# Kernel optimization log

Measured on AMD Instinct MI355X. Metric: run time of the kernel, lower is better.

Reference implementation:

```python
import jax, jax.numpy as jnp
import numpy as np

B, T, D, H, L = 4, 2048, 256, 4, 2
HD = D // H
VOCAB, MAX_BITS, MLP_H = 32, 64, 64


def setup_inputs() -> dict:
    key = jax.random.key(0)
    ks = jax.random.split(key, 20)
    s = 0.02
    n = lambda k, shp: (jax.random.normal(k, shp, jnp.float32) * s)
    inp = {
        'tokens': jax.random.randint(ks[0], (B, T), 0, VOCAB),
        'embed': n(ks[1], (VOCAB, D)),
        'ln1_w': jnp.ones((L, D)), 'ln1_b': jnp.zeros((L, D)),
        'qkv_w': n(ks[2], (L, D, 3 * D)), 'qkv_b': jnp.zeros((L, 3 * D)),
        'proj_w': n(ks[3], (L, D, D)), 'proj_b': jnp.zeros((L, D)),
        'ln2_w': jnp.ones((L, D)), 'ln2_b': jnp.zeros((L, D)),
        'ffn1_w': n(ks[4], (L, D, 4 * D)), 'ffn1_b': jnp.zeros((L, 4 * D)),
        'ffn2_w': n(ks[5], (L, 4 * D, D)), 'ffn2_b': jnp.zeros((L, D)),
        'lnf_w': jnp.ones((D,)), 'lnf_b': jnp.zeros((D,)),
        'out_queries': n(ks[6], (MAX_BITS * 2, D)),
        'outp_w': n(ks[7], (D, 1)), 'outp_b': jnp.zeros((1,)),
        'mlp_w1': n(ks[8], (3, MLP_H)), 'mlp_b1': jnp.zeros((MLP_H,)),
        'mlp_w2': n(ks[9], (MLP_H, MLP_H)), 'mlp_b2': jnp.zeros((MLP_H,)),
        'mlp_w3': n(ks[10], (MLP_H, 2)), 'mlp_b3': jnp.zeros((2,)),
    }
    return inp


def _layernorm(x, w, b, eps=1e-5):
    mu = jnp.mean(x, axis=-1, keepdims=True)
    var = jnp.mean(jnp.square(x - mu), axis=-1, keepdims=True)
    return (x - mu) * jax.lax.rsqrt(var + eps) * w + b


def _rope_tables(t_len, hd):
    inv_freq = 1.0 / (10000.0 ** (jnp.arange(0, hd, 2, dtype=jnp.float32) / hd))
    freqs = jnp.outer(jnp.arange(t_len, dtype=jnp.float32), inv_freq)  # [T, hd/2]
    emb = jnp.concatenate([freqs, freqs], axis=-1)                     # [T, hd]
    return jnp.cos(emb)[None, :, None, :], jnp.sin(emb)[None, :, None, :]


def _rotate_half(x):
    x1, x2 = x[..., : x.shape[-1] // 2], x[..., x.shape[-1] // 2:]
    return jnp.concatenate([-x2, x1], axis=-1)


def _attention(x, qkv_w, qkv_b, proj_w, proj_b):
    b, t, c = x.shape
    qkv = (x @ qkv_w + qkv_b).reshape(b, t, 3, H, HD)
    q, k, v = qkv[:, :, 0], qkv[:, :, 1], qkv[:, :, 2]  # [B,T,H,HD]
    cos, sin = _rope_tables(t, HD)
    q = q * cos + _rotate_half(q) * sin
    k = k * cos + _rotate_half(k) * sin
    scores = jnp.einsum('bthd,bshd->bhts', q, k) / jnp.sqrt(jnp.float32(HD))
    causal = jnp.tril(jnp.ones((t, t), dtype=bool))
    scores = jnp.where(causal, scores, -jnp.inf)
    attn = jax.nn.softmax(scores, axis=-1)
    out = jnp.einsum('bhts,bshd->bthd', attn, v).reshape(b, t, c)
    return out @ proj_w + proj_b


def reference(tokens, embed, ln1_w, ln1_b, qkv_w, qkv_b, proj_w, proj_b,
              ln2_w, ln2_b, ffn1_w, ffn1_b, ffn2_w, ffn2_b, lnf_w, lnf_b,
              out_queries, outp_w, outp_b,
              mlp_w1, mlp_b1, mlp_w2, mlp_b2, mlp_w3, mlp_b3):
    x = embed[tokens]  # [B,T,D]
    for l in range(L):
        x = x + _attention(_layernorm(x, ln1_w[l], ln1_b[l]),
                           qkv_w[l], qkv_b[l], proj_w[l], proj_b[l])
        h = _layernorm(x, ln2_w[l], ln2_b[l])
        h = jax.nn.gelu(h @ ffn1_w[l] + ffn1_b[l], approximate=False)
        x = x + (h @ ffn2_w[l] + ffn2_b[l])
    x = _layernorm(x, lnf_w, lnf_b)
    # query cross-attention for bit-pair selection
    q_scores = jnp.einsum('qd,btd->bqt', out_queries, x) / jnp.sqrt(jnp.float32(D))
    q_attn = jax.nn.softmax(q_scores, axis=-1)           # [B, 2*MAX_BITS, T]
    selected = jnp.einsum('bqt,btd->bqd', q_attn, x)
    bits = jax.nn.sigmoid((selected @ outp_w + outp_b)[..., 0])
    pairs = bits.reshape(-1, MAX_BITS, 2)                # [B, MAX_BITS, 2]

    # sequential full-adder over bits
    def step(carry, ab):  # carry [B], ab [B,2]
        z = jnp.concatenate([ab, carry[:, None]], axis=-1)  # [B,3]
        h = jax.nn.relu(z @ mlp_w1 + mlp_b1)
        h = jax.nn.relu(h @ mlp_w2 + mlp_b2)
        o = jax.nn.sigmoid(h @ mlp_w3 + mlp_b3)
        return o[:, 1], o[:, 0]

    carry0 = jnp.zeros((pairs.shape[0],), jnp.float32)
    carry, sum_bits = jax.lax.scan(step, carry0, jnp.swapaxes(pairs, 0, 1))
    sum_all = jnp.concatenate([sum_bits.T, carry[:, None]], axis=1)  # [B, MAX_BITS+1]
    return sum_all, pairs, q_attn
```

## Files before the change

kernel.cpp:

```cpp
#include <hip/hip_runtime.h>
#include <hip/hip_bf16.h>

#define BB 4
#define TT 2048
#define DD 256
#define HH 4
#define HDD 64
#define NROW 8192
#define NQ 128

typedef __hip_bfloat16 bf16;
typedef __attribute__((ext_vector_type(8))) short bf8v;
typedef __attribute__((ext_vector_type(4))) short bf4v;
typedef __attribute__((ext_vector_type(4))) float f4v;
typedef __attribute__((ext_vector_type(2))) unsigned int u2v;

__device__ __forceinline__ bf16 f2b(float v){ return __float2bfloat16(v); }
__device__ __forceinline__ short f2bs(float v){
    bf16 h = __float2bfloat16(v);
    return *reinterpret_cast<short*>(&h);
}
__device__ __forceinline__ float bs2f(short s){
    bf16 h = *reinterpret_cast<bf16*>(&s);
    return __bfloat162float(h);
}
__device__ __forceinline__ float rl(float v, int l){
    return __uint_as_float(__builtin_amdgcn_readlane(__float_as_uint(v), l));
}

#define DPP_ROR_ADD(v, ctrl) \
    ((v) + __int_as_float(__builtin_amdgcn_update_dpp(0, __float_as_int(v), (ctrl), 0xF, 0xF, false)))
#define DPP_ROR_MAX(v, ctrl) \
    fmaxf((v), __int_as_float(__builtin_amdgcn_update_dpp(0, __float_as_int(v), (ctrl), 0xF, 0xF, false)))

__device__ __forceinline__ void plswap16(float v, float& a, float& b){
#if __has_builtin(__builtin_amdgcn_permlane16_swap)
    u2v r = __builtin_amdgcn_permlane16_swap(__float_as_uint(v), __float_as_uint(v), false, false);
    a = __uint_as_float(r.x); b = __uint_as_float(r.y);
#else
    a = v; b = v;
    asm volatile("" : "+v"(b));
    asm("v_permlane16_swap_b32 %0, %1" : "+v"(a), "+v"(b));
#endif
}
__device__ __forceinline__ void plswap32(float v, float& a, float& b){
#if __has_builtin(__builtin_amdgcn_permlane32_swap)
    u2v r = __builtin_amdgcn_permlane32_swap(__float_as_uint(v), __float_as_uint(v), false, false);
    a = __uint_as_float(r.x); b = __uint_as_float(r.y);
#else
    a = v; b = v;
    asm volatile("" : "+v"(b));
    asm("v_permlane32_swap_b32 %0, %1" : "+v"(a), "+v"(b));
#endif
}
__device__ __forceinline__ float swap16_add(float v){ float a,b; plswap16(v,a,b); return a + b; }
__device__ __forceinline__ float swap32_add(float v){ float a,b; plswap32(v,a,b); return a + b; }
__device__ __forceinline__ float swap16_max(float v){ float a,b; plswap16(v,a,b); return fmaxf(a,b); }
__device__ __forceinline__ float swap32_max(float v){ float a,b; plswap32(v,a,b); return fmaxf(a,b); }
__device__ __forceinline__ float wsum(float v){
    v = DPP_ROR_ADD(v, 0x121); v = DPP_ROR_ADD(v, 0x122);
    v = DPP_ROR_ADD(v, 0x124); v = DPP_ROR_ADD(v, 0x128);
    v = swap16_add(v); v = swap32_add(v);
    return v;
}
__device__ __forceinline__ float wmax(float v){
    v = DPP_ROR_MAX(v, 0x121); v = DPP_ROR_MAX(v, 0x122);
    v = DPP_ROR_MAX(v, 0x124); v = DPP_ROR_MAX(v, 0x128);
    v = swap16_max(v); v = swap32_max(v);
    return v;
}

#define MFMA32(A,B,C) __builtin_amdgcn_mfma_f32_16x16x32_bf16((A),(B),(C),0,0,0)
#if __has_builtin(__builtin_amdgcn_mfma_f32_16x16x16bf16_1k)
#define MFMA16(A,B,C) __builtin_amdgcn_mfma_f32_16x16x16bf16_1k((A),(B),(C),0,0,0)
#else
__device__ __forceinline__ f4v mfma16_asm(bf4v a, bf4v b, f4v c){
    f4v d;
    asm("v_mfma_f32_16x16x16_bf16 %0, %1, %2, %3" : "=v"(d) : "v"(a), "v"(b), "v"(c));
    return d;
}
#define MFMA16(A,B,C) mfma16_asm((A),(B),(C))
#endif

__global__ __launch_bounds__(256) void k_embln(const int* __restrict__ tok,
                                               const float* __restrict__ emb,
                                               const float* __restrict__ w,
                                               const float* __restrict__ b,
                                               float* __restrict__ x,
                                               bf16* __restrict__ Y){
    int row = blockIdx.x*4 + (threadIdx.x >> 6);
    int lane = threadIdx.x & 63;
    f4v v = *(const f4v*)(emb + (long)tok[row]*DD + lane*4);
    *(f4v*)(x + (long)row*DD + lane*4) = v;
    float s  = (v[0]+v[1]) + (v[2]+v[3]);
    float s2 = (v[0]*v[0]+v[1]*v[1]) + (v[2]*v[2]+v[3]*v[3]);
    s = wsum(s); s2 = wsum(s2);
    float mu  = s * (1.0f/DD);
    float var = s2 * (1.0f/DD) - mu*mu;
    float rs  = rsqrtf(var + 1e-5f);
    f4v wv4 = *(const f4v*)(w + lane*4);
    f4v bv4 = *(const f4v*)(b + lane*4);
    bf4v o;
    #pragma unroll
    for (int i=0;i<4;i++) o[i] = f2bs((v[i]-mu)*rs*wv4[i] + bv4[i]);
    *(bf4v*)(Y + (long)row*DD + lane*4) = o;
}

__global__ __launch_bounds__(256) void k_misc(const float* __restrict__ oq, bf16* __restrict__ oqb,
                                              float* __restrict__ cosT, float* __restrict__ sinT,
                                              const float* __restrict__ w2, float* __restrict__ w2t){
    int gid = blockIdx.x*256 + threadIdx.x;
    {
        int t = gid >> 5, dd = gid & 31;
        float invf = powf(10000.0f, -(float)(2*dd)/64.0f);
        float ang = (float)t * invf;
        float sn, cs;
        sincosf(ang, &sn, &cs);
        cosT[gid] = cs; sinT[gid] = sn;
    }
    if (gid < NQ*DD) oqb[gid] = f2b(oq[gid]);
    if (gid < 4096){ int j = gid >> 6, k = gid & 63; w2t[gid] = w2[k*64 + j]; }
}

__global__ __launch_bounds__(256) void k_wtall(const float* __restrict__ qkvw,
                                               const float* __restrict__ projw,
                                               const float* __restrict__ f1w,
                                               const float* __restrict__ f2w,
                                               bf16* __restrict__ wt){
    __shared__ float t[32][33];
    int z = blockIdx.z;
    int l = z >> 2, type = z & 3;
    long L = (long)l*786432;
    int K, M; const float* src; long doff;
    if (type == 0){ K=256;  M=768;  src = qkvw + (long)l*256*768;  doff = L; }
    else if (type == 1){ K=256;  M=256;  src = projw + (long)l*256*256; doff = L + 196608; }
    else if (type == 2){ K=256;  M=1024; src = f1w  + (long)l*256*1024; doff = L + 262144; }
    else               { K=1024; M=256;  src = f2w  + (long)l*1024*256; doff = L + 524288; }
    int m0 = blockIdx.x*32, k0 = blockIdx.y*32;
    if (m0 >= M || k0 >= K) return;
    bf16* dst = wt + doff;
    int tx = threadIdx.x, ty = threadIdx.y;
    #pragma unroll
    for (int i=0;i<4;i++)
        t[ty+i*8][tx] = src[(long)(k0+ty+i*8)*M + m0 + tx];
    __syncthreads();
    #pragma unroll
    for (int i=0;i<4;i++)
        dst[(long)(m0+ty+i*8)*K + k0 + tx] = f2b(t[tx][ty+i*8]);
}

__global__ __launch_bounds__(256) void k_lnb(const float* __restrict__ X,
                                             const float* __restrict__ w,
                                             const float* __restrict__ b,
                                             bf16* __restrict__ Y){
    int row = blockIdx.x*4 + (threadIdx.x >> 6);
    int lane = threadIdx.x & 63;
    f4v v = *(const f4v*)(X + (long)row*DD + lane*4);
    float s  = (v[0]+v[1]) + (v[2]+v[3]);
    float s2 = (v[0]*v[0]+v[1]*v[1]) + (v[2]*v[2]+v[3]*v[3]);
    s = wsum(s); s2 = wsum(s2);
    float mu  = s * (1.0f/DD);
    float var = s2 * (1.0f/DD) - mu*mu;
    float rs  = rsqrtf(var + 1e-5f);
    f4v wv4 = *(const f4v*)(w + lane*4);
    f4v bv4 = *(const f4v*)(b + lane*4);
    bf4v o;
    #pragma unroll
    for (int i=0;i<4;i++) o[i] = f2bs((v[i]-mu)*rs*wv4[i] + bv4[i]);
    *(bf4v*)(Y + (long)row*DD + lane*4) = o;
}

__global__ __launch_bounds__(256) void k_lnf(const float* __restrict__ X,
                                             const float* __restrict__ w,
                                             const float* __restrict__ b,
                                             const float* __restrict__ ow,
                                             bf16* __restrict__ Yb,
                                             float* __restrict__ g){
    int row = blockIdx.x*4 + (threadIdx.x >> 6);
    int lane = threadIdx.x & 63;
    f4v v = *(const f4v*)(X + (long)row*DD + lane*4);
    float s  = (v[0]+v[1]) + (v[2]+v[3]);
    float s2 = (v[0]*v[0]+v[1]*v[1]) + (v[2]*v[2]+v[3]*v[3]);
    s = wsum(s); s2 = wsum(s2);
    float mu  = s * (1.0f/DD);
    float var = s2 * (1.0f/DD) - mu*mu;
    float rs  = rsqrtf(var + 1e-5f);
    f4v wv4 = *(const f4v*)(w + lane*4);
    f4v bv4 = *(const f4v*)(b + lane*4);
    f4v ov4 = *(const f4v*)(ow + lane*4);
    bf4v o;
    float gp = 0.f;
    #pragma unroll
    for (int i=0;i<4;i++){
        float y = (v[i]-mu)*rs*wv4[i] + bv4[i];
        o[i] = f2bs(y);
        gp += y * ov4[i];
    }
    *(bf4v*)(Yb + (long)row*DD + lane*4) = o;
    gp = wsum(gp);
    if (lane == 0) g[row] = gp;
}

__global__ __launch_bounds__(256) void k_mgemm(const bf16* __restrict__ A,
                                               const bf16* __restrict__ Wt,
                                               const float* __restrict__ bias,
                                               float* __restrict__ Cf,
                                               bf16* __restrict__ Cb,
                                               int K, int M, int mode){
    __shared__ short As[128*64];
    __shared__ short Ws[64*64];
    int tid = threadIdx.x;
    int lane = tid & 63, wv = tid >> 6;
    int n0 = blockIdx.y * 128, m0 = blockIdx.x * 64;
    int rbase = (wv >> 1) * 64, cbase = (wv & 1) * 32;
    f4v acc[4][2] = {};
    for (int k0 = 0; k0 < K; k0 += 64){
        bf8v va[4], vw[2];
        #pragma unroll
        for (int c=0;c<4;c++){
            int idx = c*256 + tid;
            va[c] = *(const bf8v*)(A + (long)(n0 + (idx>>3))*K + k0 + ((idx&7)<<3));
        }
        #pragma unroll
        for (int c=0;c<2;c++){
            int idx = c*256 + tid;
            vw[c] = *(const bf8v*)(Wt + (long)(m0 + (idx>>3))*K + k0 + ((idx&7)<<3));
        }
        __syncthreads();
        #pragma unroll
        for (int c=0;c<4;c++){
            int idx = c*256 + tid, row = idx>>3;
            *(bf8v*)&As[row*64 + (((idx&7)<<3) ^ ((row&7)<<3))] = va[c];
        }
        #pragma unroll
        for (int c=0;c<2;c++){
            int idx = c*256 + tid, row = idx>>3;
            *(bf8v*)&Ws[row*64 + (((idx&7)<<3) ^ ((row&7)<<3))] = vw[c];
        }
        __syncthreads();
        int k8 = (lane >> 4) << 3;
        #pragma unroll
        for (int h=0; h<2; h++){
            bf8v af[4], bfr[2];
            #pragma unroll
            for (int i=0;i<4;i++){
                int row = rbase + i*16 + (lane&15);
                af[i] = *(bf8v*)&As[row*64 + ((h*32 + k8) ^ ((row&7)<<3))];
            }
            #pragma unroll
            for (int j=0;j<2;j++){
                int row = cbase + j*16 + (lane&15);
                bfr[j] = *(bf8v*)&Ws[row*64 + ((h*32 + k8) ^ ((row&7)<<3))];
            }
            #pragma unroll
            for (int i=0;i<4;i++)
                #pragma unroll
                for (int j=0;j<2;j++)
                    acc[i][j] = MFMA32(af[i], bfr[j], acc[i][j]);
        }
    }
    int rq = (lane >> 4) * 4;
    int cl = lane & 15;
    #pragma unroll
    for (int i=0;i<4;i++){
        #pragma unroll
        for (int j=0;j<2;j++){
            int m = m0 + cbase + j*16 + cl;
            float bs = bias[m];
            #pragma unroll
            for (int r=0;r<4;r++){
                int n = n0 + rbase + i*16 + rq + r;
                float v = acc[i][j][r] + bs;
                long idx = (long)n*M + m;
                if (mode == 0)      Cf[idx] = v;
                else if (mode == 1) Cf[idx] += v;
                else if (mode == 2) Cb[idx] = f2b(0.5f*v*(1.0f + erff(v*0.70710678118654752f)));
                else                Cb[idx] = f2b(v);
            }
        }
    }
}

__global__ __launch_bounds__(256) void k_mgemmQKV(const bf16* __restrict__ A,
                                                  const bf16* __restrict__ Wt,
                                                  const float* __restrict__ bias,
                                                  const float* __restrict__ cosT,
                                                  const float* __restrict__ sinT,
                                                  bf16* __restrict__ qb,
                                                  bf16* __restrict__ kb,
                                                  bf16* __restrict__ vt){
    __shared__ short As[128*64];
    __shared__ short Ws[64*64];
    __shared__ short E[128][68];
    const int K = 256, M = 768;
    int tid = threadIdx.x;
    int lane = tid & 63, wv = tid >> 6;
    int n0 = blockIdx.y * 128, m0 = blockIdx.x * 64;
    int rbase = (wv >> 1) * 64, cbase = (wv & 1) * 32;
    f4v acc[4][2] = {};
    for (int k0 = 0; k0 < K; k0 += 64){
        bf8v va[4], vw[2];
        #pragma unroll
        for (int c=0;c<4;c++){
            int idx = c*256 + tid;
            va[c] = *(const bf8v*)(A + (long)(n0 + (idx>>3))*K + k0 + ((idx&7)<<3));
        }
        #pragma unroll
        for (int c=0;c<2;c++){
            int idx = c*256 + tid;
            vw[c] = *(const bf8v*)(Wt + (long)(m0 + (idx>>3))*K + k0 + ((idx&7)<<3));
        }
        __syncthreads();
        #pragma unroll
        for (int c=0;c<4;c++){
            int idx = c*256 + tid, row = idx>>3;
            *(bf8v*)&As[row*64 + (((idx&7)<<3) ^ ((row&7)<<3))] = va[c];
        }
        #pragma unroll
        for (int c=0;c<2;c++){
            int idx = c*256 + tid, row = idx>>3;
            *(bf8v*)&Ws[row*64 + (((idx&7)<<3) ^ ((row&7)<<3))] = vw[c];
        }
        __syncthreads();
        int k8 = (lane >> 4) << 3;
        #pragma unroll
        for (int h=0; h<2; h++){
            bf8v af[4], bfr[2];
            #pragma unroll
            for (int i=0;i<4;i++){
                int row = rbase + i*16 + (lane&15);
                af[i] = *(bf8v*)&As[row*64 + ((h*32 + k8) ^ ((row&7)<<3))];
            }
            #pragma unroll
            for (int j=0;j<2;j++){
                int row = cbase + j*16 + (lane&15);
                bfr[j] = *(bf8v*)&Ws[row*64 + ((h*32 + k8) ^ ((row&7)<<3))];
            }
            #pragma unroll
            for (int i=0;i<4;i++)
                #pragma unroll
                for (int j=0;j<2;j++)
                    acc[i][j] = MFMA32(af[i], bfr[j], acc[i][j]);
        }
    }
    int rq = (lane >> 4) * 4;
    int cl = lane & 15;
    #pragma unroll
    for (int i=0;i<4;i++){
        #pragma unroll
        for (int j=0;j<2;j++){
            int cc = cbase + j*16 + cl;
            float bs = bias[m0 + cc];
            #pragma unroll
            for (int r=0;r<4;r++)
                E[rbase + i*16 + rq + r][cc] = f2bs(acc[i][j][r] + bs);
        }
    }
    __syncthreads();
    int part = m0 >> 8;
    int h = (m0 >> 6) & 3;
    int b = n0 >> 11;
    int t0 = n0 & 2047;
    int bh = b*HH + h;
    if (part < 2){
        bf16* dst0 = part ? kb : qb;
        int r2 = tid >> 2;
        int c0 = (tid & 3) * 16;
        int cpx = c0 ^ 32;
        #pragma unroll
        for (int half=0; half<2; half++){
            int row = half*64 + r2;
            int t = t0 + row;
            bf8v e0 = *(bf8v*)&E[row][c0];
            bf8v e1 = *(bf8v*)&E[row][c0+8];
            bf8v p0 = *(bf8v*)&E[row][cpx];
            bf8v p1 = *(bf8v*)&E[row][cpx+8];
            const float* ct = cosT + t*32;
            const float* st = sinT + t*32;
            short o[16];
            #pragma unroll
            for (int i=0;i<8;i++){
                int d = c0 + i, dd = d & 31;
                float cs = ct[dd], sn = st[dd];
                float v = bs2f(e0[i]), v2 = bs2f(p0[i]);
                o[i] = f2bs((d < 32) ? (v*cs - v2*sn) : (v*cs + v2*sn));
            }
            #pragma unroll
            for (int i=0;i<8;i++){
                int d = c0 + 8 + i, dd = d & 31;
                float cs = ct[dd], sn = st[dd];
                float v = bs2f(e1[i]), v2 = bs2f(p1[i]);
                o[8+i] = f2bs((d < 32) ? (v*cs - v2*sn) : (v*cs + v2*sn));
            }
            short* dp = (short*)dst0 + ((long)bh*TT + t)*64 + c0;
            *(bf8v*)dp     = *(bf8v*)&o[0];
            *(bf8v*)(dp+8) = *(bf8v*)&o[8];
        }
    } else {
        int tIdx0 = t0 >> 6;
        int d  = (tid & 127) >> 1;
        int k0 = (tid & 1) * 32;
        int tt = tid >> 7;
        short o[32];
        #pragma unroll
        for (int k=0;k<32;k++) o[k] = E[tt*64 + k0 + k][d];
        short* dp = (short*)vt + (((long)bh*32 + tIdx0 + tt)*64 + d)*64 + k0;
        *(bf8v*)dp      = *(bf8v*)&o[0];
        *(bf8v*)(dp+8)  = *(bf8v*)&o[8];
        *(bf8v*)(dp+16) = *(bf8v*)&o[16];
        *(bf8v*)(dp+24) = *(bf8v*)&o[24];
    }
}

__global__ __launch_bounds__(256) void k_fattn(const bf16* __restrict__ qb,
                                               const bf16* __restrict__ kb,
                                               const bf16* __restrict__ vt,
                                               bf16* __restrict__ ob){
    __shared__ short Ks[2][64][72];
    __shared__ short Vs[2][64][68];
    int bh = blockIdx.y;
    int qt = (int)(gridDim.x - 1) - (int)blockIdx.x;
    int tid = threadIdx.x;
    int lane = tid & 63, w = tid >> 6;
    int col = lane & 15, quad = lane >> 4;
    int q0 = qt*64 + w*16;
    const bf16* qp = qb + ((long)bh*TT + q0 + col)*64 + quad*8;
    bf8v bq0 = *(const bf8v*)(qp);
    bf8v bq1 = *(const bf8v*)(qp + 32);
    f4v oc[4] = {};
    float lsum = 0.f;
    int qglob = q0 + col;
    int srow = tid >> 2, sc0 = (tid & 3) * 16;
    const short* kgb = (const short*)kb + ((long)bh*TT + srow)*64 + sc0;
    const short* vgb = (const short*)vt + (((long)bh*32)*64 + srow)*64 + sc0;

    bf8v pk0 = *(const bf8v*)kgb;
    bf8v pk1 = *(const bf8v*)(kgb + 8);
    bf8v pv0 = *(const bf8v*)vgb;
    bf8v pv1 = *(const bf8v*)(vgb + 8);
    *(bf8v*)&Ks[0][srow][sc0]     = pk0;
    *(bf8v*)&Ks[0][srow][sc0 + 8] = pk1;
    *(bf8v*)&Vs[0][srow][sc0]     = pv0;
    *(bf8v*)&Vs[0][srow][sc0 + 8] = pv1;

    int buf = 0;
    for (int kt=0; kt<=qt; kt++){
        __syncthreads();
        bool more = (kt < qt);
        if (more){
            const short* kg = kgb + (long)(kt+1)*4096;
            const short* vg = vgb + (long)(kt+1)*4096;
            pk0 = *(const bf8v*)kg;
            pk1 = *(const bf8v*)(kg + 8);
            pv0 = *(const bf8v*)vg;
            pv1 = *(const bf8v*)(vg + 8);
        }
        bool diag = (kt == qt);
        int ntmax = diag ? w : 3;
        bf4v bp[4];
        #pragma unroll
        for (int nt=0; nt<4; nt++){
            if (nt > ntmax) continue;
            bf8v ka0 = *(const bf8v*)&Ks[buf][nt*16 + col][quad*8];
            bf8v ka1 = *(const bf8v*)&Ks[buf][nt*16 + col][32 + quad*8];
            f4v st = {};
            st = MFMA32(ka0, bq0, st);
            st = MFMA32(ka1, bq1, st);
            int key0 = kt*64 + nt*16 + quad*4;
            bf4v pb;
            #pragma unroll
            for (int r=0; r<4; r++){
                float e = __expf(st[r]*0.125f);
                if (diag && (key0 + r > qglob)) e = 0.f;
                lsum += e;
                pb[r] = f2bs(e);
            }
            bp[nt] = pb;
        }
        #pragma unroll
        for (int dt=0; dt<4; dt++){
            #pragma unroll
            for (int nt=0; nt<4; nt++){
                if (nt > ntmax) continue;
                bf4v va = *(const bf4v*)&Vs[buf][dt*16 + col][nt*16 + quad*4];
                oc[dt] = MFMA16(va, bp[nt], oc[dt]);
            }
        }
        if (more){
            *(bf8v*)&Ks[buf^1][srow][sc0]     = pk0;
            *(bf8v*)&Ks[buf^1][srow][sc0 + 8] = pk1;
            *(bf8v*)&Vs[buf^1][srow][sc0]     = pv0;
            *(bf8v*)&Vs[buf^1][srow][sc0 + 8] = pv1;
        }
        buf ^= 1;
    }
    lsum += __shfl_xor(lsum, 16, 64);
    lsum += __shfl_xor(lsum, 32, 64);
    float linv = 1.0f / lsum;

    int b = bh / HH, h = bh % HH;
    long obase = ((long)b*TT + q0 + col)*DD + h*64 + quad*4;
    #pragma unroll
    for (int dt=0; dt<4; dt++){
        bf4v o4;
        #pragma unroll
        for (int r=0; r<4; r++) o4[r] = f2bs(oc[dt][r]*linv);
        *(bf4v*)(ob + obase + dt*16) = o4;
    }
}

__global__ __launch_bounds__(256) void k_score(const bf16* __restrict__ oqb,
                                               const bf16* __restrict__ xfb,
                                               float* __restrict__ S){
    int b = blockIdx.y, t0 = blockIdx.x*64;
    int tid = threadIdx.x, lane = tid & 63, w = tid >> 6;
    int col = lane & 15, quad = lane >> 4, k8 = quad << 3;
    const bf16* xb = xfb + (long)b*TT*DD;
    f4v acc[2][4] = {};
    #pragma unroll
    for (int ko=0; ko<8; ko++){
        int kk = ko*32 + k8;
        bf8v a0 = *(const bf8v*)(oqb + (long)(w*32 +      col)*DD + kk);
        bf8v a1 = *(const bf8v*)(oqb + (long)(w*32 + 16 + col)*DD + kk);
        #pragma unroll
        for (int bt=0; bt<4; bt++){
            bf8v bv = *(const bf8v*)(xb + (long)(t0 + bt*16 + col)*DD + kk);
            acc[0][bt] = MFMA32(a0, bv, acc[0][bt]);
            acc[1][bt] = MFMA32(a1, bv, acc[1][bt]);
        }
    }
    #pragma unroll
    for (int qt2=0; qt2<2; qt2++){
        #pragma unroll
        for (int bt=0; bt<4; bt++){
            #pragma unroll
            for (int r=0; r<4; r++){
                int q = w*32 + qt2*16 + quad*4 + r;
                S[((long)b*NQ + q)*TT + t0 + bt*16 + col] = acc[qt2][bt][r]*0.0625f;
            }
        }
    }
}

__global__ __launch_bounds__(256) void k_psoft(const float* __restrict__ S,
                                               const float* __restrict__ g,
                                               const float* __restrict__ obias,
                                               float* __restrict__ out_qattn,
                                               float* __restrict__ out_pairs,
                                               float* __restrict__ bits){
    __shared__ float cmax[4], cs[4], cg[4];
    int bq = blockIdx.x, b = bq >> 7;
    int tid = threadIdx.x, wv = tid >> 6, lane = tid & 63;
    const f4v* S4 = (const f4v*)(S + (long)bq*TT);
    f4v s0 = S4[tid], s1 = S4[tid + 256];
    float lmax = fmaxf(fmaxf(fmaxf(s0[0],s0[1]), fmaxf(s0[2],s0[3])),
                       fmaxf(fmaxf(s1[0],s1[1]), fmaxf(s1[2],s1[3])));
    lmax = wmax(lmax);
    if (lane == 0) cmax[wv] = lmax;
    __syncthreads();
    float m = fmaxf(fmaxf(cmax[0],cmax[1]), fmaxf(cmax[2],cmax[3]));
    const f4v* g4 = (const f4v*)(g + (long)b*TT);
    f4v gv0 = g4[tid], gv1 = g4[tid + 256];
    f4v e0, e1;
    #pragma unroll
    for (int i=0;i<4;i++){ e0[i] = __expf(s0[i]-m); e1[i] = __expf(s1[i]-m); }
    float lsum = (e0[0]+e0[1]+e0[2]+e0[3]) + (e1[0]+e1[1]+e1[2]+e1[3]);
    float gdot = (e0[0]*gv0[0]+e0[1]*gv0[1]+e0[2]*gv0[2]+e0[3]*gv0[3])
               + (e1[0]*gv1[0]+e1[1]*gv1[1]+e1[2]*gv1[2]+e1[3]*gv1[3]);
    lsum = wsum(lsum); gdot = wsum(gdot);
    if (lane == 0){ cs[wv] = lsum; cg[wv] = gdot; }
    __syncthreads();
    float Lr = (cs[0]+cs[1]) + (cs[2]+cs[3]);
    float G  = (cg[0]+cg[1]) + (cg[2]+cg[3]);
    float inv = 1.0f / Lr;
    f4v* out4 = (f4v*)(out_qattn + (long)bq*TT);
    out4[tid]       = e0 * inv;
    out4[tid + 256] = e1 * inv;
    if (tid == 0){
        float bit = 1.0f/(1.0f + expf(-(G*inv + obias[0])));
        bits[bq] = bit;
        out_pairs[bq] = bit;
    }
}

__global__ __launch_bounds__(64) void k_scan(const float* __restrict__ bits,
                                             const float* __restrict__ w1, const float* __restrict__ b1,
                                             const float* __restrict__ w2t, const float* __restrict__ b2,
                                             const float* __restrict__ w3, const float* __restrict__ b3,
                                             float* __restrict__ out_sum){
    __shared__ __align__(16) float h1s[2][64];
    int b = blockIdx.x, lane = threadIdx.x;
    float w1c0 = w1[lane], w1c1 = w1[64 + lane], w1c2 = w1[128 + lane];
    float b1v = b1[lane], b2v = b2[lane];
    float w3c0 = w3[lane*2 + 0], w3c1 = w3[lane*2 + 1];
    float b30 = b3[0], b31 = b3[1];
    const f4v* wrow = (const f4v*)(w2t + (long)lane*64);
    f4v c0v = wrow[0],  c1v = wrow[1],  c2v = wrow[2],  c3v = wrow[3],
        c4v = wrow[4],  c5v = wrow[5],  c6v = wrow[6],  c7v = wrow[7],
        c8v = wrow[8],  c9v = wrow[9],  cav = wrow[10], cbv = wrow[11],
        ccv = wrow[12], cdv = wrow[13], cev = wrow[14], cfv = wrow[15];
    float z0v = bits[b*128 + lane*2 + 0];
    float z1v = bits[b*128 + lane*2 + 1];
    float carry = 0.f;
    float a1 = rl(z0v, 0)*w1c0 + rl(z1v, 0)*w1c1 + b1v;
    for (int step=0; step<64; step++){
        float h1 = fmaxf(carry*w1c2 + a1, 0.f);
        float* hb = h1s[step & 1];
        hb[lane] = h1;
        __syncthreads();
        if (step < 63){
            a1 = rl(z0v, step+1)*w1c0 + rl(z1v, step+1)*w1c1 + b1v;
        }
        const f4v* hv = (const f4v*)hb;
        f4v va = hv[0]*c0v,  vb = hv[1]*c1v,  vc = hv[2]*c2v,   vd = hv[3]*c3v;
        va += hv[4]*c4v;   vb += hv[5]*c5v;   vc += hv[6]*c6v;   vd += hv[7]*c7v;
        va += hv[8]*c8v;   vb += hv[9]*c9v;   vc += hv[10]*cav;  vd += hv[11]*cbv;
        va += hv[12]*ccv;  vb += hv[13]*cdv;  vc += hv[14]*cev;  vd += hv[15]*cfv;
        f4v vs = (va + vb) + (vc + vd);
        float h2 = fmaxf(((vs[0] + vs[1]) + (vs[2] + vs[3])) + b2v, 0.f);
        float t0 = h2*w3c0, t1 = h2*w3c1;
        t0 = DPP_ROR_ADD(t0, 0x121); t1 = DPP_ROR_ADD(t1, 0x121);
        t0 = DPP_ROR_ADD(t0, 0x122); t1 = DPP_ROR_ADD(t1, 0x122);
        t0 = DPP_ROR_ADD(t0, 0x124); t1 = DPP_ROR_ADD(t1, 0x124);
        t0 = DPP_ROR_ADD(t0, 0x128); t1 = DPP_ROR_ADD(t1, 0x128);
        t0 = swap16_add(t0); t1 = swap16_add(t1);
        t0 = swap32_add(t0); t1 = swap32_add(t1);
        float o0 = 1.0f/(1.0f + __expf(-(t0 + b30)));
        carry    = 1.0f/(1.0f + __expf(-(t1 + b31)));
        if (lane == 0) out_sum[b*65 + step] = o0;
    }
    if (lane == 0) out_sum[b*65 + 64] = carry;
}

extern "C" void kernel_launch(void* const* d_in, const int* in_sizes, int n_in,
                              void* d_out, int out_size, void* d_ws, size_t ws_size,
                              hipStream_t stream){
    const int*   tok   = (const int*)d_in[0];
    const float* emb   = (const float*)d_in[1];
    const float* ln1w  = (const float*)d_in[2];
    const float* ln1b  = (const float*)d_in[3];
    const float* qkvw  = (const float*)d_in[4];
    const float* qkvb  = (const float*)d_in[5];
    const float* projw = (const float*)d_in[6];
    const float* projb = (const float*)d_in[7];
    const float* ln2w  = (const float*)d_in[8];
    const float* ln2b  = (const float*)d_in[9];
    const float* f1w   = (const float*)d_in[10];
    const float* f1b   = (const float*)d_in[11];
    const float* f2w   = (const float*)d_in[12];
    const float* f2bb  = (const float*)d_in[13];
    const float* lnfw  = (const float*)d_in[14];
    const float* lnfb  = (const float*)d_in[15];
    const float* oq    = (const float*)d_in[16];
    const float* ow    = (const float*)d_in[17];
    const float* obias = (const float*)d_in[18];
    const float* w1    = (const float*)d_in[19];
    const float* b1    = (const float*)d_in[20];
    const float* w2    = (const float*)d_in[21];
    const float* b2    = (const float*)d_in[22];
    const float* w3    = (const float*)d_in[23];
    const float* b3    = (const float*)d_in[24];
    float* out = (float*)d_out;

    const long MB = 1048576;
    char* W = (char*)d_ws;
    float* x     = (float*)(W);
    bf16*  attnb = (bf16*)(W + 8*MB);
    bf16*  hb    = (bf16*)(W + 16*MB);
    bf16*  qb    = (bf16*)(W + 32*MB);
    bf16*  kb    = (bf16*)(W + 36*MB);
    bf16*  vt    = (bf16*)(W + 44*MB);
    bf16*  xnb   = (bf16*)(W + 48*MB);
    bf16*  wt    = (bf16*)(W + 52*MB);
    float* bits  = (float*)(W + 55*MB);
    bf16*  oqb   = (bf16*)(W + 56*MB);
    float* cosT  = (float*)(W + 57*MB);
    float* sinT  = cosT + 65536;
    float* w2t   = (float*)(W + 58*MB);
    bf16*  xfb   = (bf16*)(W + 32*MB);
    float* g     = (float*)(W + 36*MB);
    float* S     = (float*)(W + 40*MB);

    k_wtall<<<dim3(32, 32, 8), dim3(32,8), 0, stream>>>(qkvw, projw, f1w, f2w, wt);
    k_misc<<<256, 256, 0, stream>>>(oq, oqb, cosT, sinT, w2, w2t);

    k_embln<<<NROW/4, 256, 0, stream>>>(tok, emb, ln1w, ln1b, x, xnb);
    for (int l=0; l<2; l++){
        long L = (long)l*786432;
        if (l) k_lnb<<<NROW/4, 256, 0, stream>>>(x, ln1w + l*DD, ln1b + l*DD, xnb);
        k_mgemmQKV<<<dim3(768/64, 64), 256, 0, stream>>>(
            xnb, wt + L, qkvb + l*768, cosT, sinT, qb, kb, vt);
        k_fattn<<<dim3(TT/64, BB*HH), 256, 0, stream>>>(qb, kb, vt, attnb);
        k_mgemm<<<dim3(256/64, 64), 256, 0, stream>>>(
            attnb, wt + L + 196608, projb + l*DD, x, (bf16*)0, 256, 256, 1);
        k_lnb<<<NROW/4, 256, 0, stream>>>(x, ln2w + l*DD, ln2b + l*DD, xnb);
        k_mgemm<<<dim3(1024/64, 64), 256, 0, stream>>>(
            xnb, wt + L + 262144, f1b + l*1024, (float*)0, hb, 256, 1024, 2);
        k_mgemm<<<dim3(256/64, 64), 256, 0, stream>>>(
            hb, wt + L + 524288, f2bb + l*DD, x, (bf16*)0, 1024, 256, 1);
    }
    k_lnf<<<NROW/4, 256, 0, stream>>>(x, lnfw, lnfb, ow, xfb, g);
    k_score<<<dim3(TT/64, BB), 256, 0, stream>>>(oqb, xfb, S);
    k_psoft<<<BB*NQ, 256, 0, stream>>>(S, g, obias, out + 772, out + 260, bits);
    k_scan<<<4, 64, 0, stream>>>(bits, w1, b1, w2t, b2, w3, b3, out);
}
```

Baseline: 379.7 us.

## Double-buffer LDS in generic GEMM and fold misc setup kernel into weight transpose

The generic MFMA GEMM now uses two LDS buffers and register-prefetches the next K tile right after the barrier, so global loads for tile k+1 overlap the MFMAs on tile k and one barrier per iteration goes away. The separate k_misc launch (RoPE tables, query cast, w2 transpose) becomes an extra z-slice of the weight-transpose kernel, saving one kernel launch. Doubling the LDS footprint may reduce occupancy.

Result: no change. 377.5 us (-0.6%).

```diff
diff --git a/kernel.cpp b/kernel.cpp
--- a/kernel.cpp
+++ b/kernel.cpp
@@ -106,29 +106,30 @@
     *(bf4v*)(Y + (long)row*DD + lane*4) = o;
 }
 
-__global__ __launch_bounds__(256) void k_misc(const float* __restrict__ oq, bf16* __restrict__ oqb,
-                                              float* __restrict__ cosT, float* __restrict__ sinT,
-                                              const float* __restrict__ w2, float* __restrict__ w2t){
-    int gid = blockIdx.x*256 + threadIdx.x;
-    {
-        int t = gid >> 5, dd = gid & 31;
-        float invf = powf(10000.0f, -(float)(2*dd)/64.0f);
-        float ang = (float)t * invf;
-        float sn, cs;
-        sincosf(ang, &sn, &cs);
-        cosT[gid] = cs; sinT[gid] = sn;
-    }
-    if (gid < NQ*DD) oqb[gid] = f2b(oq[gid]);
-    if (gid < 4096){ int j = gid >> 6, k = gid & 63; w2t[gid] = w2[k*64 + j]; }
-}
-
 __global__ __launch_bounds__(256) void k_wtall(const float* __restrict__ qkvw,
                                                const float* __restrict__ projw,
                                                const float* __restrict__ f1w,
                                                const float* __restrict__ f2w,
-                                               bf16* __restrict__ wt){
+                                               bf16* __restrict__ wt,
+                                               const float* __restrict__ oq, bf16* __restrict__ oqb,
+                                               float* __restrict__ cosT, float* __restrict__ sinT,
+                                               const float* __restrict__ w2, float* __restrict__ w2t){
     __shared__ float t[32][33];
     int z = blockIdx.z;
+    if (z == 8){
+        int bid = blockIdx.y*32 + blockIdx.x;
+        if (bid >= 256) return;
+        int gid = bid*256 + threadIdx.y*32 + threadIdx.x;
+        int tt = gid >> 5, dd = gid & 31;
+        float invf = powf(10000.0f, -(float)(2*dd)/64.0f);
+        float ang = (float)tt * invf;
+        float sn, cs;
+        sincosf(ang, &sn, &cs);
+        cosT[gid] = cs; sinT[gid] = sn;
+        if (gid < NQ*DD) oqb[gid] = f2b(oq[gid]);
+        if (gid < 4096){ int j = gid >> 6, k = gid & 63; w2t[gid] = w2[k*64 + j]; }
+        return;
+    }
     int l = z >> 2, type = z & 3;
     long L = (long)l*786432;
     int K, M; const float* src; long doff;
@@ -207,37 +208,49 @@
                                                float* __restrict__ Cf,
                                                bf16* __restrict__ Cb,
                                                int K, int M, int mode){
-    __shared__ short As[128*64];
-    __shared__ short Ws[64*64];
+    __shared__ short As[2][128*64];
+    __shared__ short Ws[2][64*64];
     int tid = threadIdx.x;
     int lane = tid & 63, wv = tid >> 6;
     int n0 = blockIdx.y * 128, m0 = blockIdx.x * 64;
     int rbase = (wv >> 1) * 64, cbase = (wv & 1) * 32;
     f4v acc[4][2] = {};
+    bf8v va[4], vw[2];
+    #pragma unroll
+    for (int c=0;c<4;c++){
+        int idx = c*256 + tid;
+        va[c] = *(const bf8v*)(A + (long)(n0 + (idx>>3))*K + ((idx&7)<<3));
+    }
+    #pragma unroll
+    for (int c=0;c<2;c++){
+        int idx = c*256 + tid;
+        vw[c] = *(const bf8v*)(Wt + (long)(m0 + (idx>>3))*K + ((idx&7)<<3));
+    }
+    int buf = 0;
     for (int k0 = 0; k0 < K; k0 += 64){
-        bf8v va[4], vw[2];
-        #pragma unroll
-        for (int c=0;c<4;c++){
-            int idx = c*256 + tid;
-            va[c] = *(const bf8v*)(A + (long)(n0 + (idx>>3))*K + k0 + ((idx&7)<<3));
-        }
-        #pragma unroll
-        for (int c=0;c<2;c++){
-            int idx = c*256 + tid;
-            vw[c] = *(const bf8v*)(Wt + (long)(m0 + (idx>>3))*K + k0 + ((idx&7)<<3));
-        }
-        __syncthreads();
         #pragma unroll
         for (int c=0;c<4;c++){
             int idx = c*256 + tid, row = idx>>3;
-            *(bf8v*)&As[row*64 + (((idx&7)<<3) ^ ((row&7)<<3))] = va[c];
+            *(bf8v*)&As[buf][row*64 + (((idx&7)<<3) ^ ((row&7)<<3))] = va[c];
         }
         #pragma unroll
         for (int c=0;c<2;c++){
             int idx = c*256 + tid, row = idx>>3;
-            *(bf8v*)&Ws[row*64 + (((idx&7)<<3) ^ ((row&7)<<3))] = vw[c];
+            *(bf8v*)&Ws[buf][row*64 + (((idx&7)<<3) ^ ((row&7)<<3))] = vw[c];
         }
         __syncthreads();
+        if (k0 + 64 < K){
+            #pragma unroll
+            for (int c=0;c<4;c++){
+                int idx = c*256 + tid;
+                va[c] = *(const bf8v*)(A + (long)(n0 + (idx>>3))*K + k0 + 64 + ((idx&7)<<3));
+            }
+            #pragma unroll
+            for (int c=0;c<2;c++){
+                int idx = c*256 + tid;
+                vw[c] = *(const bf8v*)(Wt + (long)(m0 + (idx>>3))*K + k0 + 64 + ((idx&7)<<3));
+            }
+        }
         int k8 = (lane >> 4) << 3;
         #pragma unroll
         for (int h=0; h<2; h++){
@@ -245,12 +258,12 @@
             #pragma unroll
             for (int i=0;i<4;i++){
                 int row = rbase + i*16 + (lane&15);
-                af[i] = *(bf8v*)&As[row*64 + ((h*32 + k8) ^ ((row&7)<<3))];
+                af[i] = *(bf8v*)&As[buf][row*64 + ((h*32 + k8) ^ ((row&7)<<3))];
             }
             #pragma unroll
             for (int j=0;j<2;j++){
                 int row = cbase + j*16 + (lane&15);
-                bfr[j] = *(bf8v*)&Ws[row*64 + ((h*32 + k8) ^ ((row&7)<<3))];
+                bfr[j] = *(bf8v*)&Ws[buf][row*64 + ((h*32 + k8) ^ ((row&7)<<3))];
             }
             #pragma unroll
             for (int i=0;i<4;i++)
@@ -258,6 +271,7 @@
                 for (int j=0;j<2;j++)
                     acc[i][j] = MFMA32(af[i], bfr[j], acc[i][j]);
         }
+        buf ^= 1;
     }
     int rq = (lane >> 4) * 4;
     int cl = lane & 15;
@@ -681,8 +695,8 @@
     float* g     = (float*)(W + 36*MB);
     float* S     = (float*)(W + 40*MB);
 
-    k_wtall<<<dim3(32, 32, 8), dim3(32,8), 0, stream>>>(qkvw, projw, f1w, f2w, wt);
-    k_misc<<<256, 256, 0, stream>>>(oq, oqb, cosT, sinT, w2, w2t);
+    k_wtall<<<dim3(32, 32, 9), dim3(32,8), 0, stream>>>(qkvw, projw, f1w, f2w, wt,
+                                                        oq, oqb, cosT, sinT, w2, w2t);
 
     k_embln<<<NROW/4, 256, 0, stream>>>(tok, emb, ln1w, ln1b, x, xnb);
     for (int l=0; l<2; l++){
```
